# Performance work log

Measured on AMD Instinct MI355X. Metric: run time of the kernel, lower is better.

The kernel has to match this reference:

```python
import jax, jax.numpy as jnp
import numpy as np

B, L, E, H = 1, 2048, 1024, 16
HW = E // H  # head width = 64
SCALE = HW ** -0.5


def setup_inputs() -> dict:
    key = jax.random.key(0)
    ks = jax.random.split(key, 8)
    x = jax.random.normal(ks[0], (B, L, E), dtype=jnp.float32)
    mask = jax.random.bernoulli(ks[1], 0.9, (B, L))
    mask = mask.at[:, 0].set(True)  # guarantee at least one valid key per batch
    bias = jax.random.normal(ks[2], (B, L, L, H), dtype=jnp.float32)
    # torch nn.Linear stores weight as [out, in]; we keep that convention
    w_proj = jax.random.normal(ks[3], (3 * E, E), dtype=jnp.float32) * (E ** -0.5)
    w_o = jax.random.normal(ks[4], (E, E), dtype=jnp.float32) * (E ** -0.5)
    b_o = jax.random.normal(ks[5], (E,), dtype=jnp.float32) * 0.02
    w_g = jax.random.normal(ks[6], (E, E), dtype=jnp.float32) * (E ** -0.5)
    b_g = jax.random.normal(ks[7], (E,), dtype=jnp.float32) * 0.02
    return {"x": x, "mask": mask, "bias": bias, "w_proj": w_proj,
            "w_o": w_o, "b_o": b_o, "w_g": w_g, "b_g": b_g}


def reference(x, mask, bias, w_proj, w_o, b_o, w_g, b_g):
    # proj -> [B, L, 3E], rearrange '(h c)' with h=H so each head slice holds [q|k|v]
    t = jnp.einsum('ble,fe->blf', x, w_proj)               # [B, L, 3E]
    t = t.reshape(B, L, H, 3 * HW).transpose(0, 2, 1, 3)   # [B, H, L, 3*HW]
    q, k, v = jnp.split(t, 3, axis=-1)                     # each [B, H, L, HW]
    a = jnp.einsum('bhqc,bhkc->bhqk', SCALE * q, k)        # [B, H, L, L]
    a = a + bias.transpose(0, 3, 1, 2)                     # bias: [B,Lq,Lk,H] -> [B,H,Lq,Lk]
    a = jnp.where(mask[:, None, None, :], a, -jnp.inf)
    a = jax.nn.softmax(a, axis=-1)
    y = jnp.einsum('bhqk,bhkc->bqhc', a, v).reshape(B, L, E)
    g = jax.nn.sigmoid(jnp.einsum('ble,fe->blf', x, w_g) + b_g)
    y = g * y
    return jnp.einsum('ble,fe->blf', y, w_o) + b_o
```

## Files before the change

### kernel.cpp

```cpp
#include <hip/hip_runtime.h>
#include <stdint.h>

#define LSEQ 2048
#define EMB  1024
#define NH   16
#define HWID 64
#define SCALEF 0.125f

typedef __attribute__((ext_vector_type(4))) float  f32x4;
typedef __attribute__((ext_vector_type(8))) short  bf16x8;
typedef __attribute__((ext_vector_type(8))) unsigned short u16x8;
typedef __attribute__((ext_vector_type(4))) unsigned short u16x4;

static __device__ __forceinline__ unsigned short f2bf(float f) {
    union { float f; unsigned int u; } v; v.f = f;
    unsigned int r = (v.u + 0x7FFFu + ((v.u >> 16) & 1u)) >> 16;
    return (unsigned short)r;
}
static __device__ __forceinline__ float bf2f(unsigned short h) {
    union { unsigned int u; float f; } v; v.u = ((unsigned int)h) << 16;
    return v.f;
}

static __device__ __forceinline__ void gload_lds16(const void* g, void* l) {
    __builtin_amdgcn_global_load_lds((const __attribute__((address_space(1))) void*)g,
                                     (__attribute__((address_space(3))) void*)l,
                                     16, 0, 0);
}

__global__ __launch_bounds__(256) void convert_kernel(
    const float* __restrict__ x, const float* __restrict__ wp,
    const float* __restrict__ wg, const float* __restrict__ wo,
    unsigned short* __restrict__ xb, unsigned short* __restrict__ wcat,
    unsigned short* __restrict__ wob)
{
    const int NX  = (LSEQ * EMB) / 4;
    const int NWP = (3 * EMB * EMB) / 4;
    const int NWG = (EMB * EMB) / 4;
    const int NWO = (EMB * EMB) / 4;
    const int total = NX + NWP + NWG + NWO;
    for (int i = blockIdx.x * blockDim.x + threadIdx.x; i < total;
         i += gridDim.x * blockDim.x) {
        const float4* src; unsigned short* dst; int j;
        if (i < NX)                  { src = (const float4*)x;  dst = xb;                  j = i; }
        else if (i < NX + NWP)       { src = (const float4*)wp; dst = wcat;                j = i - NX; }
        else if (i < NX + NWP + NWG) { src = (const float4*)wg; dst = wcat + 3 * EMB * EMB; j = i - NX - NWP; }
        else                         { src = (const float4*)wo; dst = wob;                 j = i - NX - NWP - NWG; }
        float4 v = src[j];
        u16x4 o;
        o.x = f2bf(v.x); o.y = f2bf(v.y); o.z = f2bf(v.z); o.w = f2bf(v.w);
        *(u16x4*)(dst + (size_t)j * 4) = o;
    }
}

__global__ void decode_mask_kernel(const unsigned char* __restrict__ mask,
                                   float* __restrict__ mbias)
{
    __shared__ int cnt;
    if (threadIdx.x == 0) cnt = 0;
    __syncthreads();
    int c = 0;
    for (int i = threadIdx.x; i < LSEQ; i += 256) c += (mask[i] != 0);
    atomicAdd(&cnt, c);
    __syncthreads();
    bool isbyte = cnt > LSEQ / 2;
    for (int k = threadIdx.x; k < LSEQ; k += 256) {
        bool v;
        if (isbyte) v = (mask[k] != 0);
        else        v = ((mask[4*k] | mask[4*k+1] | mask[4*k+2] | mask[4*k+3]) != 0);
        mbias[k] = v ? 0.f : -1e30f;
    }
}

#define BM 128
#define BN 128
#define BK 64

__global__ __launch_bounds__(256) void gemm_bt_kernel(
    const unsigned short* __restrict__ A, const unsigned short* __restrict__ B,
    void* __restrict__ Cout, const float* __restrict__ biasN,
    int M, int N, int K, int epi)
{
    __shared__ unsigned short As[BM][BK];
    __shared__ unsigned short Bs[BN][BK];
    const int tid  = threadIdx.x;
    const int lane = tid & 63;
    const int w    = tid >> 6;
    const int wr   = w >> 1, wc = w & 1;
    const int row0 = blockIdx.y * BM;
    const int col0 = blockIdx.x * BN;
    const int lr = lane & 15;
    const int lg = lane >> 4;

    f32x4 acc[4][4];
    const f32x4 zf = {0.f, 0.f, 0.f, 0.f};
#pragma unroll
    for (int m = 0; m < 4; ++m)
#pragma unroll
        for (int n = 0; n < 4; ++n) acc[m][n] = zf;

    const char* Ab = (const char*)(A + (size_t)row0 * K);
    const char* Bb = (const char*)(B + (size_t)col0 * K);
    const int Kb = K * 2;

    for (int kt = 0; kt < K; kt += BK) {
#pragma unroll
        for (int i = 0; i < 4; ++i) {
            int o = (i * 256 + tid) * 16;
            int r = o >> 7, cb = o & 127;
            gload_lds16(Ab + (size_t)r * Kb + kt * 2 + cb, (char*)As + o);
        }
#pragma unroll
        for (int i = 0; i < 4; ++i) {
            int o = (i * 256 + tid) * 16;
            int r = o >> 7, cb = o & 127;
            gload_lds16(Bb + (size_t)r * Kb + kt * 2 + cb, (char*)Bs + o);
        }
        __syncthreads();
#pragma unroll
        for (int kk = 0; kk < 2; ++kk) {
            bf16x8 af[4], bfr[4];
            const int lk = kk * 32 + lg * 8;
#pragma unroll
            for (int m = 0; m < 4; ++m) af[m]  = *(const bf16x8*)&As[wr * 64 + m * 16 + lr][lk];
#pragma unroll
            for (int n = 0; n < 4; ++n) bfr[n] = *(const bf16x8*)&Bs[wc * 64 + n * 16 + lr][lk];
#pragma unroll
            for (int m = 0; m < 4; ++m)
#pragma unroll
                for (int n = 0; n < 4; ++n)
                    acc[m][n] = __builtin_amdgcn_mfma_f32_16x16x32_bf16(af[m], bfr[n], acc[m][n], 0, 0, 0);
        }
        __syncthreads();
    }

#pragma unroll
    for (int m = 0; m < 4; ++m)
#pragma unroll
        for (int n = 0; n < 4; ++n) {
            const int col = col0 + wc * 64 + n * 16 + lr;
#pragma unroll
            for (int r = 0; r < 4; ++r) {
                const int row = row0 + wr * 64 + m * 16 + lg * 4 + r;
                if (epi == 0)
                    ((unsigned short*)Cout)[(size_t)row * N + col] = f2bf(acc[m][n][r]);
                else
                    ((float*)Cout)[(size_t)row * N + col] = acc[m][n][r] + biasN[col];
            }
        }
}

__global__ __launch_bounds__(256) void rearrange_kernel(
    const unsigned short* __restrict__ T, const float* __restrict__ bg,
    unsigned short* __restrict__ Qh, unsigned short* __restrict__ Kh,
    unsigned short* __restrict__ G)
{
    const int l = blockIdx.x;
    const int t = threadIdx.x;
    const unsigned short* trow = T + (size_t)l * 4096;
    {
        const int tt = t & 127;
        const int h  = tt >> 3;
        const int c0 = (tt & 7) * 8;
        const bool isq = (t < 128);
        const int srcoff = h * 192 + (isq ? 0 : 64) + c0;
        u16x8 v = *(const u16x8*)(trow + srcoff);
        if (isq) {
#pragma unroll
            for (int j = 0; j < 8; ++j) v[j] = f2bf(bf2f(v[j]) * SCALEF);
        }
        unsigned short* dst = (isq ? Qh : Kh) + ((size_t)h * LSEQ + l) * HWID + c0;
        *(u16x8*)dst = v;
    }
    {
        const int f0 = t * 4;
        float4 b4 = *(const float4*)(bg + f0);
        u16x4 tv = *(const u16x4*)(trow + 3 * EMB + f0);
        u16x4 o;
        o.x = f2bf(1.f / (1.f + __expf(-(bf2f(tv.x) + b4.x))));
        o.y = f2bf(1.f / (1.f + __expf(-(bf2f(tv.y) + b4.y))));
        o.z = f2bf(1.f / (1.f + __expf(-(bf2f(tv.z) + b4.z))));
        o.w = f2bf(1.f / (1.f + __expf(-(bf2f(tv.w) + b4.w))));
        *(u16x4*)(G + (size_t)l * EMB + f0) = o;
    }
}

__global__ __launch_bounds__(256) void vtrans_kernel(
    const unsigned short* __restrict__ T, unsigned short* __restrict__ VT)
{
    __shared__ unsigned short tile[64][72];
    const int h  = blockIdx.x & 15;
    const int lt = blockIdx.x >> 4;
    const int l0 = lt * 64;
    const int t  = threadIdx.x;
    {
        const int i = t >> 2, c0 = (t & 3) * 16;
        const unsigned short* src = T + (size_t)(l0 + i) * 4096 + h * 192 + 128;
        *(u16x8*)&tile[i][c0]     = *(const u16x8*)(src + c0);
        *(u16x8*)&tile[i][c0 + 8] = *(const u16x8*)(src + c0 + 8);
    }
    __syncthreads();
    {
        const int c = t >> 2, j0 = (t & 3) * 16;
        unsigned short* dst = VT + ((size_t)h * HWID + c) * LSEQ + l0 + j0;
        u16x8 a, b;
#pragma unroll
        for (int j = 0; j < 8; ++j) a[j] = tile[j0 + j][c];
#pragma unroll
        for (int j = 0; j < 8; ++j) b[j] = tile[j0 + 8 + j][c];
        *(u16x8*)dst       = a;
        *(u16x8*)(dst + 8) = b;
    }
}

#define NT 32

__global__ __launch_bounds__(256) void attn_kernel(
    const unsigned short* __restrict__ Qh, const unsigned short* __restrict__ Kh,
    const unsigned short* __restrict__ VT, const float* __restrict__ bias,
    const float* __restrict__ mbias,
    float* __restrict__ Op, float* __restrict__ Ml)
{
    __shared__ float bias_s[3][4][16 * 33];
    __shared__ unsigned short ps[4][16][40];
    __shared__ float mk[1024];

    const int tid  = threadIdx.x;
    const int lane = tid & 63;
    const int w    = tid >> 6;
    const int bi   = blockIdx.x;
    const int hg   = bi >> 8;
    const int u    = bi & 255;
    const int qsub = u >> 1;
    const int sp   = u & 1;
    const int h4   = hg * 4;
    const int h    = h4 + w;
    const int q0   = qsub * 16;
    const int koff = sp * 1024;
    const int lr   = lane & 15;
    const int lg   = lane >> 4;

    const unsigned short* Qbase = Qh + ((size_t)h * LSEQ + q0) * HWID;
    const bf16x8 qa0 = *(const bf16x8*)(Qbase + lr * HWID + lg * 8);
    const bf16x8 qa1 = *(const bf16x8*)(Qbase + lr * HWID + 32 + lg * 8);

    const unsigned short* Kbase = Kh + ((size_t)h * LSEQ + koff) * HWID;
    const unsigned short* Vbase = VT + (size_t)h * HWID * LSEQ + koff;
    const char* bias_base = (const char*)bias;

    auto loadBias = [&](int t, float4* bv) {
        const int kg = koff + t * 32;
#pragma unroll
        for (int p2 = 0; p2 < 2; ++p2) {
            const int jj = p2 * 256 + tid;
            const int q = jj >> 5, k = jj & 31;
            bv[p2] = *(const float4*)(bias_base +
                     (((size_t)(q0 + q) * LSEQ + kg + k) * NH + h4) * 4);
        }
    };
    auto writeBias = [&](int slot, const float4* bv) {
        float (*dst)[16 * 33] = bias_s[slot];
#pragma unroll
        for (int p2 = 0; p2 < 2; ++p2) {
            const int jj = p2 * 256 + tid;
            const int q = jj >> 5, k = jj & 31;
            const int idx = q * 33 + k;
            dst[0][idx] = bv[p2].x;
            dst[1][idx] = bv[p2].y;
            dst[2][idx] = bv[p2].z;
            dst[3][idx] = bv[p2].w;
        }
    };

    bf16x8 ones;
#pragma unroll
    for (int j2 = 0; j2 < 8; ++j2) ones[j2] = (short)0x3F80;

    float mrow[4];
    f32x4 acc[4], lsum;
    const f32x4 zf = {0.f, 0.f, 0.f, 0.f};
#pragma unroll
    for (int r = 0; r < 4; ++r) mrow[r] = -1e30f;
#pragma unroll
    for (int c = 0; c < 4; ++c) acc[c] = zf;
    lsum = zf;

    float4 tmp[2], bwA[2], bwB[2];
    loadBias(0, tmp);
    loadBias(1, bwB);
    {
        float4 mv = *(const float4*)(mbias + koff + tid * 4);
        *(float4*)&mk[tid * 4] = mv;
    }
    __syncthreads();
    writeBias(0, tmp);
    asm volatile("s_waitcnt lgkmcnt(0)" ::: "memory");
    __builtin_amdgcn_s_barrier();

    auto body = [&](int t, float4 (&bwL)[2], float4 (&bwW)[2]) {
        const int kg = t * 32;

        bf16x8 kb[2][2];
#pragma unroll
        for (int t2 = 0; t2 < 2; ++t2) {
            const unsigned short* kp = Kbase + (size_t)(kg + t2 * 16 + lr) * HWID + lg * 8;
            kb[t2][0] = *(const bf16x8*)kp;
            kb[t2][1] = *(const bf16x8*)(kp + 32);
        }
        bf16x8 vb[4];
#pragma unroll
        for (int ct = 0; ct < 4; ++ct)
            vb[ct] = *(const bf16x8*)(Vbase + (size_t)(ct * 16 + lr) * LSEQ + kg + lg * 8);
        asm volatile("" ::: "memory");

        if (t + 2 < NT) loadBias(t + 2, bwL);
        asm volatile("" ::: "memory");

        f32x4 S[2];
#pragma unroll
        for (int t2 = 0; t2 < 2; ++t2) {
            f32x4 s = zf;
            s = __builtin_amdgcn_mfma_f32_16x16x32_bf16(qa0, kb[t2][0], s, 0, 0, 0);
            s = __builtin_amdgcn_mfma_f32_16x16x32_bf16(qa1, kb[t2][1], s, 0, 0, 0);
            S[t2] = s;
        }

        const float* bpl = bias_s[t % 3][w];
        const float m0 = mk[kg + lr];
        const float m1 = mk[kg + 16 + lr];
        float sc0[4], sc1[4], lm[4];
#pragma unroll
        for (int r = 0; r < 4; ++r) {
            const int qrow = (lg * 4 + r) * 33;
            sc0[r] = S[0][r] + bpl[qrow + lr] + m0;
            sc1[r] = S[1][r] + bpl[qrow + 16 + lr] + m1;
            lm[r] = fmaxf(sc0[r], sc1[r]);
        }
        const float need = fmaxf(fmaxf(lm[0] - mrow[0], lm[1] - mrow[1]),
                                 fmaxf(lm[2] - mrow[2], lm[3] - mrow[3]));
        if (!__all(need <= 8.0f)) {
            float rm[4];
#pragma unroll
            for (int r = 0; r < 4; ++r) rm[r] = lm[r];
#pragma unroll
            for (int off = 1; off < 16; off <<= 1)
#pragma unroll
                for (int r = 0; r < 4; ++r)
                    rm[r] = fmaxf(rm[r], __shfl_xor(rm[r], off, 64));
            float sf[4];
#pragma unroll
            for (int r = 0; r < 4; ++r) {
                const float mn = fmaxf(mrow[r], rm[r]);
                sf[r] = __expf(mrow[r] - mn);
                mrow[r] = mn;
            }
#pragma unroll
            for (int ct = 0; ct < 4; ++ct)
#pragma unroll
                for (int r = 0; r < 4; ++r) acc[ct][r] *= sf[r];
#pragma unroll
            for (int r = 0; r < 4; ++r) lsum[r] *= sf[r];
        }

        float p0[4], p1[4];
#pragma unroll
        for (int r = 0; r < 4; ++r) {
            p0[r] = __expf(sc0[r] - mrow[r]);
            p1[r] = __expf(sc1[r] - mrow[r]);
        }

#pragma unroll
        for (int r = 0; r < 4; ++r) {
            ps[w][lg * 4 + r][lr]      = f2bf(p0[r]);
            ps[w][lg * 4 + r][16 + lr] = f2bf(p1[r]);
        }
        const bf16x8 pa = *(const bf16x8*)&ps[w][lr][lg * 8];

#pragma unroll
        for (int ct = 0; ct < 4; ++ct)
            acc[ct] = __builtin_amdgcn_mfma_f32_16x16x32_bf16(pa, vb[ct], acc[ct], 0, 0, 0);
        lsum = __builtin_amdgcn_mfma_f32_16x16x32_bf16(pa, ones, lsum, 0, 0, 0);

        asm volatile("" ::: "memory");
        __builtin_amdgcn_s_barrier();
        if (t + 1 < NT) writeBias((t + 1) % 3, bwW);
        asm volatile("s_waitcnt lgkmcnt(0)" ::: "memory");
        __builtin_amdgcn_s_barrier();
    };

#pragma unroll 1
    for (int tt = 0; tt < NT; tt += 2) {
        body(tt,     bwA, bwB);
        body(tt + 1, bwB, bwA);
    }

    const size_t rowb = ((size_t)sp * NH + h) * LSEQ;
#pragma unroll
    for (int ct = 0; ct < 4; ++ct)
#pragma unroll
        for (int r = 0; r < 4; ++r) {
            const int q = q0 + lg * 4 + r;
            Op[(rowb + q) * HWID + ct * 16 + lr] = acc[ct][r];
        }
    if (lr == 0) {
#pragma unroll
        for (int r = 0; r < 4; ++r) {
            const int q = q0 + lg * 4 + r;
            Ml[(rowb + q) * 2 + 0] = mrow[r];
            Ml[(rowb + q) * 2 + 1] = lsum[r];
        }
    }
}

__global__ __launch_bounds__(256) void combine_kernel(
    const float* __restrict__ Op, const float* __restrict__ Ml,
    const unsigned short* __restrict__ G, unsigned short* __restrict__ Yb)
{
    const int t   = threadIdx.x;
    const int c   = t & 63;
    const int row = blockIdx.x * 4 + (t >> 6);
    const int h   = row >> 11;
    const int q   = row & (LSEQ - 1);
    const size_t r0 = (size_t)h * LSEQ + q;
    const size_t r1 = ((size_t)NH + h) * LSEQ + q;
    const float m0 = Ml[r0 * 2 + 0], l0 = Ml[r0 * 2 + 1];
    const float m1 = Ml[r1 * 2 + 0], l1 = Ml[r1 * 2 + 1];
    const float mx = fmaxf(m0, m1);
    const float a0 = __expf(m0 - mx), a1 = __expf(m1 - mx);
    const float inv = 1.f / (l0 * a0 + l1 * a1);
    const float o0 = Op[r0 * HWID + c];
    const float o1 = Op[r1 * HWID + c];
    const float y = (o0 * a0 + o1 * a1) * inv;
    const int e = h * HWID + c;
    const float g = bf2f(G[(size_t)q * EMB + e]);
    Yb[(size_t)q * EMB + e] = f2bf(y * g);
}

extern "C" void kernel_launch(void* const* d_in, const int* in_sizes, int n_in,
                              void* d_out, int out_size, void* d_ws, size_t ws_size,
                              hipStream_t stream) {
    const float*         x      = (const float*)d_in[0];
    const unsigned char* mask   = (const unsigned char*)d_in[1];
    const float*         bias   = (const float*)d_in[2];
    const float*         w_proj = (const float*)d_in[3];
    const float*         w_o    = (const float*)d_in[4];
    const float*         b_o    = (const float*)d_in[5];
    const float*         w_g    = (const float*)d_in[6];
    const float*         b_g    = (const float*)d_in[7];
    float* out = (float*)d_out;
    (void)in_sizes; (void)n_in; (void)out_size; (void)ws_size;

    char* p = (char*)d_ws;
    auto alloc = [&](size_t bytes) {
        char* r = p; p += (bytes + 255) & ~(size_t)255; return r;
    };
    unsigned short* xb    = (unsigned short*)alloc((size_t)LSEQ * EMB * 2);
    unsigned short* wcat  = (unsigned short*)alloc((size_t)4 * EMB * EMB * 2);
    unsigned short* wob   = (unsigned short*)alloc((size_t)EMB * EMB * 2);
    unsigned short* T     = (unsigned short*)alloc((size_t)LSEQ * 4096 * 2);
    unsigned short* Qh    = (unsigned short*)alloc((size_t)NH * LSEQ * HWID * 2);
    unsigned short* Kh    = (unsigned short*)alloc((size_t)NH * LSEQ * HWID * 2);
    unsigned short* VT    = (unsigned short*)alloc((size_t)NH * HWID * LSEQ * 2);
    unsigned short* G     = (unsigned short*)alloc((size_t)LSEQ * EMB * 2);
    unsigned short* Yb    = (unsigned short*)alloc((size_t)LSEQ * EMB * 2);
    float*          mb    = (float*)alloc((size_t)LSEQ * 4);
    float*          Op    = (float*)alloc((size_t)2 * NH * LSEQ * HWID * 4);
    float*          Ml    = (float*)alloc((size_t)2 * NH * LSEQ * 2 * 4);

    convert_kernel<<<1024, 256, 0, stream>>>(x, w_proj, w_g, w_o, xb, wcat, wob);
    decode_mask_kernel<<<1, 256, 0, stream>>>(mask, mb);
    gemm_bt_kernel<<<dim3(4096 / BN, LSEQ / BM), 256, 0, stream>>>(
        xb, wcat, (void*)T, nullptr, LSEQ, 4096, EMB, 0);
    rearrange_kernel<<<LSEQ, 256, 0, stream>>>(T, b_g, Qh, Kh, G);
    vtrans_kernel<<<NH * (LSEQ / 64), 256, 0, stream>>>(T, VT);
    attn_kernel<<<1024, 256, 0, stream>>>(Qh, Kh, VT, bias, mb, Op, Ml);
    combine_kernel<<<NH * LSEQ / 4, 256, 0, stream>>>(Op, Ml, G, Yb);
    gemm_bt_kernel<<<dim3(EMB / BN, LSEQ / BM), 256, 0, stream>>>(
        Yb, wob, (void*)out, b_o, LSEQ, EMB, EMB, 1);
}
```

Baseline: 289.8 us.

## Double attention block to 32 query rows, double-buffer bias, prefetch K tiles

The attention kernel now runs 512 threads (8 waves) per block covering 32 query rows × 4 heads, halving the grid. The bias staging drops from triple to double buffering in LDS. K fragments are prefetched one tile ahead into registers alongside the bias prefetch. Bias loads stay coalesced over a larger tile, and the block count per launch is halved. In exchange there are fewer blocks, higher register pressure from the K prefetch, and the barrier-heavy loop now has more waves per sync.

```diff
diff --git a/kernel.cpp b/kernel.cpp
--- a/kernel.cpp
+++ b/kernel.cpp
@@ -215,32 +215,35 @@
 
 #define NT 32
 
-__global__ __launch_bounds__(256) void attn_kernel(
+__global__ __launch_bounds__(512, 4) void attn_kernel(
     const unsigned short* __restrict__ Qh, const unsigned short* __restrict__ Kh,
     const unsigned short* __restrict__ VT, const float* __restrict__ bias,
     const float* __restrict__ mbias,
     float* __restrict__ Op, float* __restrict__ Ml)
 {
-    __shared__ float bias_s[3][4][16 * 33];
-    __shared__ unsigned short ps[4][16][40];
+    __shared__ float bias_s[2][4][1056];
+    __shared__ unsigned short ps[8][16][40];
     __shared__ float mk[1024];
 
     const int tid  = threadIdx.x;
     const int lane = tid & 63;
     const int w    = tid >> 6;
     const int bi   = blockIdx.x;
-    const int hg   = bi >> 8;
-    const int u    = bi & 255;
-    const int qsub = u >> 1;
+    const int hg   = bi >> 7;
+    const int u    = bi & 127;
+    const int qt   = u >> 1;
     const int sp   = u & 1;
     const int h4   = hg * 4;
-    const int h    = h4 + w;
-    const int q0   = qsub * 16;
+    const int h    = h4 + (w & 3);
+    const int q0b  = qt * 32;
+    const int q0w  = q0b + (w >> 2) * 16;
     const int koff = sp * 1024;
     const int lr   = lane & 15;
     const int lg   = lane >> 4;
-
-    const unsigned short* Qbase = Qh + ((size_t)h * LSEQ + q0) * HWID;
+    const int hloc = w & 3;
+    const int qloc = (w >> 2) * 16 + lg * 4;
+
+    const unsigned short* Qbase = Qh + ((size_t)h * LSEQ + q0w) * HWID;
     const bf16x8 qa0 = *(const bf16x8*)(Qbase + lr * HWID + lg * 8);
     const bf16x8 qa1 = *(const bf16x8*)(Qbase + lr * HWID + 32 + lg * 8);
 
@@ -252,17 +255,17 @@
         const int kg = koff + t * 32;
 #pragma unroll
         for (int p2 = 0; p2 < 2; ++p2) {
-            const int jj = p2 * 256 + tid;
+            const int jj = p2 * 512 + tid;
             const int q = jj >> 5, k = jj & 31;
             bv[p2] = *(const float4*)(bias_base +
-                     (((size_t)(q0 + q) * LSEQ + kg + k) * NH + h4) * 4);
+                     (((size_t)(q0b + q) * LSEQ + kg + k) * NH + h4) * 4);
         }
     };
     auto writeBias = [&](int slot, const float4* bv) {
-        float (*dst)[16 * 33] = bias_s[slot];
+        float (*dst)[1056] = bias_s[slot];
 #pragma unroll
         for (int p2 = 0; p2 < 2; ++p2) {
-            const int jj = p2 * 256 + tid;
+            const int jj = p2 * 512 + tid;
             const int q = jj >> 5, k = jj & 31;
             const int idx = q * 33 + k;
             dst[0][idx] = bv[p2].x;
@@ -285,53 +288,62 @@
     for (int c = 0; c < 4; ++c) acc[c] = zf;
     lsum = zf;
 
-    float4 tmp[2], bwA[2], bwB[2];
+    auto loadK = [&](int t, bf16x8 (&kb)[2][2]) {
+        const int kg = t * 32;
+#pragma unroll
+        for (int t2 = 0; t2 < 2; ++t2) {
+            const unsigned short* kp = Kbase + (size_t)(kg + t2 * 16 + lr) * HWID + lg * 8;
+            kb[t2][0] = *(const bf16x8*)kp;
+            kb[t2][1] = *(const bf16x8*)(kp + 32);
+        }
+    };
+
+    float4 tmp[2], bvA[2], bvB[2];
+    bf16x8 kbA[2][2], kbB[2][2];
     loadBias(0, tmp);
-    loadBias(1, bwB);
+    loadBias(1, bvB);
+    loadK(0, kbA);
     {
-        float4 mv = *(const float4*)(mbias + koff + tid * 4);
-        *(float4*)&mk[tid * 4] = mv;
+        float2 mv = *(const float2*)(mbias + koff + tid * 2);
+        *(float2*)&mk[tid * 2] = mv;
     }
     __syncthreads();
     writeBias(0, tmp);
     asm volatile("s_waitcnt lgkmcnt(0)" ::: "memory");
     __builtin_amdgcn_s_barrier();
 
-    auto body = [&](int t, float4 (&bwL)[2], float4 (&bwW)[2]) {
+    auto body = [&](int t, int slot, bf16x8 (&kbCur)[2][2], bf16x8 (&kbNxt)[2][2],
+                    float4 (&bvRecv)[2], float4 (&bvWrite)[2]) {
         const int kg = t * 32;
-
-        bf16x8 kb[2][2];
-#pragma unroll
-        for (int t2 = 0; t2 < 2; ++t2) {
-            const unsigned short* kp = Kbase + (size_t)(kg + t2 * 16 + lr) * HWID + lg * 8;
-            kb[t2][0] = *(const bf16x8*)kp;
-            kb[t2][1] = *(const bf16x8*)(kp + 32);
-        }
+        const int tn1 = (t + 1 < NT) ? t + 1 : NT - 1;
+        const int tn2 = (t + 2 < NT) ? t + 2 : NT - 1;
+
         bf16x8 vb[4];
 #pragma unroll
         for (int ct = 0; ct < 4; ++ct)
             vb[ct] = *(const bf16x8*)(Vbase + (size_t)(ct * 16 + lr) * LSEQ + kg + lg * 8);
         asm volatile("" ::: "memory");
-
-        if (t + 2 < NT) loadBias(t + 2, bwL);
+        loadBias(tn2, bvRecv);
+        asm volatile("" ::: "memory");
+        loadK(tn1, kbNxt);
         asm volatile("" ::: "memory");
 
         f32x4 S[2];
 #pragma unroll
         for (int t2 = 0; t2 < 2; ++t2) {
             f32x4 s = zf;
-            s = __builtin_amdgcn_mfma_f32_16x16x32_bf16(qa0, kb[t2][0], s, 0, 0, 0);
-            s = __builtin_amdgcn_mfma_f32_16x16x32_bf16(qa1, kb[t2][1], s, 0, 0, 0);
+            s = __builtin_amdgcn_mfma_f32_16x16x32_bf16(qa0, kbCur[t2][0], s, 0, 0, 0);
+            s = __builtin_amdgcn_mfma_f32_16x16x32_bf16(qa1, kbCur[t2][1], s, 0, 0, 0);
             S[t2] = s;
         }
 
-        const float* bpl = bias_s[t % 3][w];
+        const float* bpl = bias_s[slot][hloc];
         const float m0 = mk[kg + lr];
         const float m1 = mk[kg + 16 + lr];
         float sc0[4], sc1[4], lm[4];
 #pragma unroll
         for (int r = 0; r < 4; ++r) {
-            const int qrow = (lg * 4 + r) * 33;
+            const int qrow = (qloc + r) * 33;
             sc0[r] = S[0][r] + bpl[qrow + lr] + m0;
             sc1[r] = S[1][r] + bpl[qrow + 16 + lr] + m1;
             lm[r] = fmaxf(sc0[r], sc1[r]);
@@ -383,15 +395,15 @@
 
         asm volatile("" ::: "memory");
         __builtin_amdgcn_s_barrier();
-        if (t + 1 < NT) writeBias((t + 1) % 3, bwW);
+        writeBias(slot ^ 1, bvWrite);
         asm volatile("s_waitcnt lgkmcnt(0)" ::: "memory");
         __builtin_amdgcn_s_barrier();
     };
 
 #pragma unroll 1
     for (int tt = 0; tt < NT; tt += 2) {
-        body(tt,     bwA, bwB);
-        body(tt + 1, bwB, bwA);
+        body(tt,     0, kbA, kbB, bvA, bvB);
+        body(tt + 1, 1, kbB, kbA, bvB, bvA);
     }
 
     const size_t rowb = ((size_t)sp * NH + h) * LSEQ;
@@ -399,13 +411,13 @@
     for (int ct = 0; ct < 4; ++ct)
 #pragma unroll
         for (int r = 0; r < 4; ++r) {
-            const int q = q0 + lg * 4 + r;
+            const int q = q0w + lg * 4 + r;
             Op[(rowb + q) * HWID + ct * 16 + lr] = acc[ct][r];
         }
     if (lr == 0) {
 #pragma unroll
         for (int r = 0; r < 4; ++r) {
-            const int q = q0 + lg * 4 + r;
+            const int q = q0w + lg * 4 + r;
             Ml[(rowb + q) * 2 + 0] = mrow[r];
             Ml[(rowb + q) * 2 + 1] = lsum[r];
         }
@@ -473,7 +485,7 @@
         xb, wcat, (void*)T, nullptr, LSEQ, 4096, EMB, 0);
     rearrange_kernel<<<LSEQ, 256, 0, stream>>>(T, b_g, Qh, Kh, G);
     vtrans_kernel<<<NH * (LSEQ / 64), 256, 0, stream>>>(T, VT);
-    attn_kernel<<<1024, 256, 0, stream>>>(Qh, Kh, VT, bias, mb, Op, Ml);
+    attn_kernel<<<512, 512, 0, stream>>>(Qh, Kh, VT, bias, mb, Op, Ml);
     combine_kernel<<<NH * LSEQ / 4, 256, 0, stream>>>(Op, Ml, G, Yb);
     gemm_bt_kernel<<<dim3(EMB / BN, LSEQ / BM), 256, 0, stream>>>(
         Yb, wob, (void*)out, b_o, LSEQ, EMB, EMB, 1);
```

Measured after the change: 293.2 us. Within noise of the previous version (+1.2%).

## Process all 16 heads per attention block to read full bias rows contiguously

Applied to the files above, without the earlier changes.

The attention kernel now launches 256 blocks of 1024 threads, one wave per head, so each block covers all 16 heads for a 16-query by 1024-key tile. Bias loads become two contiguous float4 reads per thread covering the full 64-byte head row, instead of 16-byte strided slices gathered by four separate head-group blocks. The bias LDS ring shrinks to double buffering, one barrier per iteration is dropped, and K fragments are now prefetched one tile ahead. The trade-offs are fewer, larger blocks with more LDS each (lower occupancy flexibility, and 256 blocks may underfill the GPU), plus higher register pressure from the extra K buffers.

```diff
diff --git a/kernel.cpp b/kernel.cpp
--- a/kernel.cpp
+++ b/kernel.cpp
@@ -215,26 +215,22 @@
 
 #define NT 32
 
-__global__ __launch_bounds__(256) void attn_kernel(
+__global__ __launch_bounds__(1024) void attn_kernel(
     const unsigned short* __restrict__ Qh, const unsigned short* __restrict__ Kh,
     const unsigned short* __restrict__ VT, const float* __restrict__ bias,
     const float* __restrict__ mbias,
     float* __restrict__ Op, float* __restrict__ Ml)
 {
-    __shared__ float bias_s[3][4][16 * 33];
-    __shared__ unsigned short ps[4][16][40];
+    __shared__ float bias_s[2][16][576];
+    __shared__ unsigned short ps[16][16][40];
     __shared__ float mk[1024];
 
     const int tid  = threadIdx.x;
     const int lane = tid & 63;
     const int w    = tid >> 6;
-    const int bi   = blockIdx.x;
-    const int hg   = bi >> 8;
-    const int u    = bi & 255;
-    const int qsub = u >> 1;
-    const int sp   = u & 1;
-    const int h4   = hg * 4;
-    const int h    = h4 + w;
+    const int qsub = blockIdx.x >> 1;
+    const int sp   = blockIdx.x & 1;
+    const int h    = w;
     const int q0   = qsub * 16;
     const int koff = sp * 1024;
     const int lr   = lane & 15;
@@ -246,29 +242,34 @@
 
     const unsigned short* Kbase = Kh + ((size_t)h * LSEQ + koff) * HWID;
     const unsigned short* Vbase = VT + (size_t)h * HWID * LSEQ + koff;
-    const char* bias_base = (const char*)bias;
+
+    const int li   = tid >> 1;
+    const int bq   = li >> 5;
+    const int bk   = li & 31;
+    const int half = tid & 1;
+    const float* bsrc0 = bias +
+        ((size_t)(q0 + bq) * LSEQ + (koff + bk)) * NH + half * 8;
+    const int bidx = bq * 36 + bk;
 
     auto loadBias = [&](int t, float4* bv) {
-        const int kg = koff + t * 32;
-#pragma unroll
-        for (int p2 = 0; p2 < 2; ++p2) {
-            const int jj = p2 * 256 + tid;
-            const int q = jj >> 5, k = jj & 31;
-            bv[p2] = *(const float4*)(bias_base +
-                     (((size_t)(q0 + q) * LSEQ + kg + k) * NH + h4) * 4);
-        }
+        const float* src = bsrc0 + (size_t)t * 32 * NH;
+        bv[0] = *(const float4*)(src);
+        bv[1] = *(const float4*)(src + 4);
     };
     auto writeBias = [&](int slot, const float4* bv) {
-        float (*dst)[16 * 33] = bias_s[slot];
-#pragma unroll
-        for (int p2 = 0; p2 < 2; ++p2) {
-            const int jj = p2 * 256 + tid;
-            const int q = jj >> 5, k = jj & 31;
-            const int idx = q * 33 + k;
-            dst[0][idx] = bv[p2].x;
-            dst[1][idx] = bv[p2].y;
-            dst[2][idx] = bv[p2].z;
-            dst[3][idx] = bv[p2].w;
+#pragma unroll
+        for (int j = 0; j < 4; ++j) {
+            bias_s[slot][half * 8 + j][bidx]     = ((const float*)&bv[0])[j];
+            bias_s[slot][half * 8 + 4 + j][bidx] = ((const float*)&bv[1])[j];
+        }
+    };
+    auto loadK = [&](int t, bf16x8 (&kb)[2][2]) {
+        const int kgl = t * 32;
+#pragma unroll
+        for (int t2 = 0; t2 < 2; ++t2) {
+            const unsigned short* kp = Kbase + (size_t)(kgl + t2 * 16 + lr) * HWID + lg * 8;
+            kb[t2][0] = *(const bf16x8*)kp;
+            kb[t2][1] = *(const bf16x8*)(kp + 32);
         }
     };
 
@@ -285,53 +286,47 @@
     for (int c = 0; c < 4; ++c) acc[c] = zf;
     lsum = zf;
 
-    float4 tmp[2], bwA[2], bwB[2];
-    loadBias(0, tmp);
-    loadBias(1, bwB);
-    {
-        float4 mv = *(const float4*)(mbias + koff + tid * 4);
-        *(float4*)&mk[tid * 4] = mv;
-    }
+    float4 bv[2];
+    bf16x8 kbA[2][2], kbB[2][2];
+    loadBias(0, bv);
+    loadK(0, kbA);
+    mk[tid] = mbias[koff + tid];
     __syncthreads();
-    writeBias(0, tmp);
+    writeBias(0, bv);
     asm volatile("s_waitcnt lgkmcnt(0)" ::: "memory");
     __builtin_amdgcn_s_barrier();
 
-    auto body = [&](int t, float4 (&bwL)[2], float4 (&bwW)[2]) {
-        const int kg = t * 32;
-
-        bf16x8 kb[2][2];
-#pragma unroll
-        for (int t2 = 0; t2 < 2; ++t2) {
-            const unsigned short* kp = Kbase + (size_t)(kg + t2 * 16 + lr) * HWID + lg * 8;
-            kb[t2][0] = *(const bf16x8*)kp;
-            kb[t2][1] = *(const bf16x8*)(kp + 32);
-        }
+    const unsigned short (*psb)[40] = nullptr; (void)psb;
+
+    auto body = [&](int t, bf16x8 (&kbCur)[2][2], bf16x8 (&kbNxt)[2][2]) {
+        const int kgl = t * 32;
+
         bf16x8 vb[4];
 #pragma unroll
         for (int ct = 0; ct < 4; ++ct)
-            vb[ct] = *(const bf16x8*)(Vbase + (size_t)(ct * 16 + lr) * LSEQ + kg + lg * 8);
+            vb[ct] = *(const bf16x8*)(Vbase + (size_t)(ct * 16 + lr) * LSEQ + kgl + lg * 8);
         asm volatile("" ::: "memory");
-
-        if (t + 2 < NT) loadBias(t + 2, bwL);
+        if (t + 1 < NT) loadK(t + 1, kbNxt);
+        asm volatile("" ::: "memory");
+        if (t + 1 < NT) loadBias(t + 1, bv);
         asm volatile("" ::: "memory");
 
         f32x4 S[2];
 #pragma unroll
         for (int t2 = 0; t2 < 2; ++t2) {
             f32x4 s = zf;
-            s = __builtin_amdgcn_mfma_f32_16x16x32_bf16(qa0, kb[t2][0], s, 0, 0, 0);
-            s = __builtin_amdgcn_mfma_f32_16x16x32_bf16(qa1, kb[t2][1], s, 0, 0, 0);
+            s = __builtin_amdgcn_mfma_f32_16x16x32_bf16(qa0, kbCur[t2][0], s, 0, 0, 0);
+            s = __builtin_amdgcn_mfma_f32_16x16x32_bf16(qa1, kbCur[t2][1], s, 0, 0, 0);
             S[t2] = s;
         }
 
-        const float* bpl = bias_s[t % 3][w];
-        const float m0 = mk[kg + lr];
-        const float m1 = mk[kg + 16 + lr];
+        const float* bpl = &bias_s[t & 1][w][0];
+        const float m0 = mk[kgl + lr];
+        const float m1 = mk[kgl + 16 + lr];
         float sc0[4], sc1[4], lm[4];
 #pragma unroll
         for (int r = 0; r < 4; ++r) {
-            const int qrow = (lg * 4 + r) * 33;
+            const int qrow = (lg * 4 + r) * 36;
             sc0[r] = S[0][r] + bpl[qrow + lr] + m0;
             sc1[r] = S[1][r] + bpl[qrow + 16 + lr] + m1;
             lm[r] = fmaxf(sc0[r], sc1[r]);
@@ -381,17 +376,15 @@
             acc[ct] = __builtin_amdgcn_mfma_f32_16x16x32_bf16(pa, vb[ct], acc[ct], 0, 0, 0);
         lsum = __builtin_amdgcn_mfma_f32_16x16x32_bf16(pa, ones, lsum, 0, 0, 0);
 
-        asm volatile("" ::: "memory");
-        __builtin_amdgcn_s_barrier();
-        if (t + 1 < NT) writeBias((t + 1) % 3, bwW);
+        if (t + 1 < NT) writeBias((t + 1) & 1, bv);
         asm volatile("s_waitcnt lgkmcnt(0)" ::: "memory");
         __builtin_amdgcn_s_barrier();
     };
 
 #pragma unroll 1
     for (int tt = 0; tt < NT; tt += 2) {
-        body(tt,     bwA, bwB);
-        body(tt + 1, bwB, bwA);
+        body(tt,     kbA, kbB);
+        body(tt + 1, kbB, kbA);
     }
 
     const size_t rowb = ((size_t)sp * NH + h) * LSEQ;
@@ -473,7 +466,7 @@
         xb, wcat, (void*)T, nullptr, LSEQ, 4096, EMB, 0);
     rearrange_kernel<<<LSEQ, 256, 0, stream>>>(T, b_g, Qh, Kh, G);
     vtrans_kernel<<<NH * (LSEQ / 64), 256, 0, stream>>>(T, VT);
-    attn_kernel<<<1024, 256, 0, stream>>>(Qh, Kh, VT, bias, mb, Op, Ml);
+    attn_kernel<<<256, 1024, 0, stream>>>(Qh, Kh, VT, bias, mb, Op, Ml);
     combine_kernel<<<NH * LSEQ / 4, 256, 0, stream>>>(Op, Ml, G, Yb);
     gemm_bt_kernel<<<dim3(EMB / BN, LSEQ / BM), 256, 0, stream>>>(
         Yb, wob, (void*)out, b_o, LSEQ, EMB, EMB, 1);
```

Result: faster. 238.0 us (-17.9%).
